# Kernel optimization log

Measured on AMD Instinct MI355X. Metric: run time of the kernel, lower is better.

## Reference

```python
import jax, jax.numpy as jnp
import numpy as np

B, T, D, H = 8, 1024, 512, 8
DK = D // H


def setup_inputs() -> dict:
    key = jax.random.key(0)
    ks = jax.random.split(key, 6)
    s = 0.02
    return {
        "inputs": jax.random.normal(ks[0], (B, T, D), jnp.float32),
        "ln1_g": jnp.ones((D,), jnp.float32),
        "ln1_b": jnp.zeros((D,), jnp.float32),
        "ln2_g": jnp.ones((D,), jnp.float32),
        "ln2_b": jnp.zeros((D,), jnp.float32),
        "W_qkv": jax.random.normal(ks[1], (3 * D, D), jnp.float32) * s,
        "W_pos": jax.random.normal(ks[2], (D, D), jnp.float32) * s,
        "W_out": jax.random.normal(ks[3], (D, D), jnp.float32) * s,
        "b_out": jnp.zeros((D,), jnp.float32),
        "pos_bias_u": jax.random.normal(ks[4], (H, DK), jnp.float32) * s,
        "pos_bias_v": jax.random.normal(ks[5], (H, DK), jnp.float32) * s,
    }


def layer_norm(x, g, b, eps=1e-5):
    mu = jnp.mean(x, axis=-1, keepdims=True)
    var = jnp.var(x, axis=-1, keepdims=True)
    return (x - mu) * jax.lax.rsqrt(var + eps) * g + b


def rel_shift(x):
    # x: (b, h, t1, t2); Transformer-XL pad-reshape-slice relative shift
    b, h, t1, t2 = x.shape
    xp = jnp.pad(x, ((0, 0), (0, 0), (0, 0), (1, 0)))  # zero col at front
    xp = xp.reshape(b, h, t2 + 1, t1)[:, :, 1:, :]
    return xp.reshape(b, h, t1, t2)


def reference(inputs, ln1_g, ln1_b, ln2_g, ln2_b, W_qkv, W_pos, W_out, b_out,
              pos_bias_u, pos_bias_v):
    b, t, d = inputs.shape
    # PositionalEmbedding: pos_seq is the literal data values inputs[0,:,0]
    pos_seq = inputs[0, :, 0]
    inv_freq = 1.0 / (10000.0 ** (jnp.arange(0, d, 2, dtype=jnp.float32) / d))
    sin_inp = pos_seq[:, None] * inv_freq[None, :]  # (T, D/2)
    pos_emb = jnp.concatenate([jnp.sin(sin_inp), jnp.cos(sin_inp)], axis=-1)  # (T, D)
    # outer layer norm, then inner layer norm inside forward_qkv
    x = layer_norm(inputs, ln1_g, ln1_b)
    xn = layer_norm(x, ln2_g, ln2_b)
    qkv = xn @ W_qkv.T  # (B, T, 3D)
    q, k, v = jnp.split(qkv, 3, axis=-1)
    q = q.reshape(b, t, H, DK)                       # (B, T, H, DK)
    k = k.reshape(b, t, H, DK).transpose(0, 2, 1, 3)  # (B, H, T, DK)
    v = v.reshape(b, t, H, DK).transpose(0, 2, 1, 3)  # (B, H, T, DK)
    p = (pos_emb @ W_pos.T).reshape(t, H, DK)         # (T, H, DK), pos batch = 1
    qu = (q + pos_bias_u).transpose(0, 2, 1, 3)       # (B, H, T, DK)
    qv = (q + pos_bias_v).transpose(0, 2, 1, 3)
    ac = jnp.einsum('bhqd,bhkd->bhqk', qu, k)
    bd = jnp.einsum('bhqd,khd->bhqk', qv, p)
    bd = rel_shift(bd)
    scores = (ac + bd) / jnp.sqrt(jnp.float32(DK))
    attn = jax.nn.softmax(scores, axis=-1)
    out = jnp.einsum('bhqk,bhkd->bqhd', attn, v).reshape(b, t, d)
    return out @ W_out.T + b_out
```

## Files before the change

kernel.cpp:

```cpp
#include <hip/hip_runtime.h>
#include <stdint.h>

#define B_ 8
#define T_ 1024
#define D_ 512
#define H_ 8
#define DK_ 64
#define M_ (B_*T_)

#define PREP_CAST_BLKS (5 * D_ * D_ / 4 / 256)
#define PREP_POS_BLKS  (T_)
#define PREP_LN_BLKS   (M_)
#define PREP_BLKS      (PREP_CAST_BLKS + PREP_POS_BLKS + PREP_LN_BLKS)

typedef unsigned short u16;
typedef __attribute__((ext_vector_type(8))) short bf16x8;
typedef __attribute__((ext_vector_type(4))) float f32x4;

static __device__ __forceinline__ u16 f2bf(float f) {
  union { float f; unsigned u; } v; v.f = f;
  unsigned r = (v.u + 0x7fffu + ((v.u >> 16) & 1u)) >> 16;
  return (u16)r;
}
static __device__ __forceinline__ u16 f2bf_ru(float f) {
  union { float f; unsigned u; } v; v.f = f;
  return (u16)((v.u + 0x8000u) >> 16);
}
static __device__ __forceinline__ float bf2f(u16 u) {
  union { unsigned u; float f; } v; v.u = ((unsigned)u) << 16;
  return v.f;
}
static __device__ __forceinline__ void async16(const u16* g, u16* l) {
  __builtin_amdgcn_global_load_lds(
      (const __attribute__((address_space(1))) void*)g,
      (__attribute__((address_space(3))) void*)l, 16, 0, 0);
}
static __device__ __forceinline__ f32x4 mfma16(bf16x8 a, bf16x8 b, f32x4 c) {
  return __builtin_amdgcn_mfma_f32_16x16x32_bf16(a, b, c, 0, 0, 0);
}

__global__ __launch_bounds__(256)
void prep_k(const float* __restrict__ wq, const float* __restrict__ wp,
            const float* __restrict__ wo, u16* __restrict__ dq,
            u16* __restrict__ dp, u16* __restrict__ dwo,
            const float* __restrict__ x, u16* __restrict__ pe,
            const float* __restrict__ g1, const float* __restrict__ b1,
            const float* __restrict__ g2, const float* __restrict__ b2,
            u16* __restrict__ xn) {
  __shared__ float red[16];
  const int blk = blockIdx.x;
  const int t = threadIdx.x;
  if (blk < PREP_CAST_BLKS) {
    const int na = 3 * D_ * D_ / 4, nb = D_ * D_ / 4;
    int i = blk * 256 + t;
    const float* s; u16* d; int j;
    if (i < na) { s = wq; d = dq; j = i; }
    else if (i < na + nb) { s = wp; d = dp; j = i - na; }
    else { s = wo; d = dwo; j = i - na - nb; }
    float4 v = ((const float4*)s)[j];
    ushort4 o;
    o.x = f2bf(v.x); o.y = f2bf(v.y); o.z = f2bf(v.z); o.w = f2bf(v.w);
    ((ushort4*)d)[j] = o;
  } else if (blk < PREP_CAST_BLKS + PREP_POS_BLKS) {
    const int tt = blk - PREP_CAST_BLKS;
    float pos = x[(size_t)tt * D_];
    float invf = expf(-(2.f * t / (float)D_) * 9.210340371976184f);
    float ang = pos * invf;
    pe[(size_t)tt * D_ + t] = f2bf(sinf(ang));
    pe[(size_t)tt * D_ + 256 + t] = f2bf(cosf(ang));
  } else {
    const int row = blk - PREP_CAST_BLKS - PREP_POS_BLKS;
    const float2 v = *(const float2*)(x + (size_t)row * D_ + t * 2);
    float a = v.x + v.y;
    float b = v.x * v.x + v.y * v.y;
    for (int off = 32; off; off >>= 1) { a += __shfl_down(a, off, 64); b += __shfl_down(b, off, 64); }
    if ((t & 63) == 0) { red[t >> 6] = a; red[8 + (t >> 6)] = b; }
    __syncthreads();
    a = red[0] + red[1] + red[2] + red[3];
    b = red[8] + red[9] + red[10] + red[11];
    float mu = a * (1.f / D_);
    float var = b * (1.f / D_) - mu * mu;
    float rs = rsqrtf(var + 1e-5f);
    const float2 g1v = *(const float2*)(g1 + t * 2);
    const float2 b1v = *(const float2*)(b1 + t * 2);
    float y0 = (v.x - mu) * rs * g1v.x + b1v.x;
    float y1 = (v.y - mu) * rs * g1v.y + b1v.y;
    __syncthreads();
    a = y0 + y1;
    b = y0 * y0 + y1 * y1;
    for (int off = 32; off; off >>= 1) { a += __shfl_down(a, off, 64); b += __shfl_down(b, off, 64); }
    if ((t & 63) == 0) { red[t >> 6] = a; red[8 + (t >> 6)] = b; }
    __syncthreads();
    a = red[0] + red[1] + red[2] + red[3];
    b = red[8] + red[9] + red[10] + red[11];
    mu = a * (1.f / D_);
    var = b * (1.f / D_) - mu * mu;
    rs = rsqrtf(var + 1e-5f);
    const float2 g2v = *(const float2*)(g2 + t * 2);
    const float2 b2v = *(const float2*)(b2 + t * 2);
    u16* o = xn + (size_t)row * D_ + t * 2;
    o[0] = f2bf((y0 - mu) * rs * g2v.x + b2v.x);
    o[1] = f2bf((y1 - mu) * rs * g2v.y + b2v.y);
  }
}

template<int MODE>
__global__ __launch_bounds__(256, 2)
void gemm_k(const u16* __restrict__ A, const u16* __restrict__ Bw,
            int M, int N, int K,
            u16* __restrict__ o0, u16* __restrict__ o1, u16* __restrict__ o2,
            float* __restrict__ fo, const float* __restrict__ bo) {
  __shared__ u16 As[2][128 * 32];
  __shared__ u16 Bs[2][128 * 32];
  const int tid = threadIdx.x;
  const int l = tid & 63, w = tid >> 6;
  const int m0 = blockIdx.x * 128, n0 = blockIdx.y * 128;
  const int wm = (w >> 1) * 64, wn = (w & 1) * 64;
  const int nk = K >> 5;

  auto stage = [&](int bufi, int kt) {
    const int row = tid >> 2;
    const int cg = ((tid & 3) ^ ((row + (row >> 2)) & 3)) * 8;
    const u16* ga = A + (size_t)(m0 + row) * K + kt * 32 + cg;
    u16* la = &As[bufi][tid * 8];
    async16(ga, la);
    async16(ga + (size_t)64 * K, la + 64 * 32);
    const u16* gb = Bw + (size_t)(n0 + row) * K + kt * 32 + cg;
    u16* lb = &Bs[bufi][tid * 8];
    async16(gb, lb);
    async16(gb + (size_t)64 * K, lb + 64 * 32);
  };

  const int fl = (((l & 15) + ((l & 15) >> 2)) & 3);
  const int coff = ((l >> 4) ^ fl) * 8;
  const int aoff = (l & 15) * 32 + coff;

  f32x4 acc[4][4] = {};
  stage(0, 0);
  for (int kt = 0; kt < nk; ++kt) {
    __syncthreads();
    if (kt + 1 < nk) stage((kt + 1) & 1, kt + 1);
    const u16* as = As[kt & 1];
    const u16* bs = Bs[kt & 1];
    bf16x8 af[4], bfr[4];
#pragma unroll
    for (int i = 0; i < 4; ++i)
      af[i] = *(const bf16x8*)&as[(wm + i * 16) * 32 + aoff];
#pragma unroll
    for (int j = 0; j < 4; ++j)
      bfr[j] = *(const bf16x8*)&bs[(wn + j * 16) * 32 + aoff];
#pragma unroll
    for (int i = 0; i < 4; ++i)
#pragma unroll
      for (int j = 0; j < 4; ++j)
        acc[i][j] = mfma16(af[i], bfr[j], acc[i][j]);
  }

#pragma unroll
  for (int i = 0; i < 4; ++i)
#pragma unroll
    for (int j = 0; j < 4; ++j) {
      const int row0 = m0 + wm + i * 16 + ((l >> 4) << 2);
      const int col = n0 + wn + j * 16 + (l & 15);
      if (MODE == 0) {
        const int sec = col >> 9, cc = col & 511;
        const int hh = cc >> 6, dk = cc & 63;
        const int bb = row0 >> 10, t0r = row0 & 1023;
        if (sec == 2) {
          ushort4 v4;
          v4.x = f2bf(acc[i][j][0]); v4.y = f2bf(acc[i][j][1]);
          v4.z = f2bf(acc[i][j][2]); v4.w = f2bf(acc[i][j][3]);
          *(ushort4*)&o2[((size_t)(bb * H_ + hh) * DK_ + dk) * T_ + t0r] = v4;
        } else {
          u16* dst = (sec == 0) ? o0 : o1;
#pragma unroll
          for (int r = 0; r < 4; ++r)
            dst[((size_t)(bb * H_ + hh) * T_ + t0r + r) * DK_ + dk] = f2bf(acc[i][j][r]);
        }
      } else if (MODE == 1) {
        const int hh = col >> 6, dk = col & 63;
#pragma unroll
        for (int r = 0; r < 4; ++r)
          o0[((size_t)hh * T_ + row0 + r) * DK_ + dk] = f2bf(acc[i][j][r]);
      } else {
#pragma unroll
        for (int r = 0; r < 4; ++r)
          fo[(size_t)(row0 + r) * D_ + col] = acc[i][j][r] + bo[col];
      }
    }
}

__global__ __launch_bounds__(256, 3)
void attn_k(const u16* __restrict__ q, const u16* __restrict__ kb,
            const u16* __restrict__ vt, const u16* __restrict__ pb,
            const float* __restrict__ bu, const float* __restrict__ bv,
            u16* __restrict__ ao) {
  __shared__ u16 k_lds[64 * 64];
  __shared__ u16 v_lds[64 * 64];
  __shared__ u16 p_lds[128 * 64];
  __shared__ u16 pscr[4][16 * 72];

  const int tid = threadIdx.x;
  const int l = tid & 63, w = tid >> 6;
  const int dd = blockIdx.x;
  const int bh = (dd & 7) * 8 + (dd >> 7);
  const int qb = (dd >> 3) & 15;
  const int q0 = qb * 64;
  const int b = bh >> 3, h = bh & 7;

  const u16* qB = q + (size_t)bh * T_ * DK_;
  const u16* kB = kb + (size_t)bh * T_ * DK_;
  const u16* vB = vt + (size_t)bh * DK_ * T_;
  const u16* pB = pb + (size_t)h * T_ * DK_;

  const float SCALE = 0.125f * 1.4426950408889634f;

  bf16x8 quf[2], qvf[2], qsf[2];
  {
    const float* buH = bu + h * DK_;
    const float* bvH = bv + h * DK_;
    const int row = q0 + w * 16 + (l & 15);
    const int row2 = (row + 1 < T_) ? row + 1 : T_ - 1;
    const int ko = (l >> 4) * 8;
    const bf16x8 qa0 = *(const bf16x8*)(qB + (size_t)row * DK_ + ko);
    const bf16x8 qa1 = *(const bf16x8*)(qB + (size_t)row * DK_ + ko + 32);
    const bf16x8 qs0 = *(const bf16x8*)(qB + (size_t)row2 * DK_ + ko);
    const bf16x8 qs1 = *(const bf16x8*)(qB + (size_t)row2 * DK_ + ko + 32);
#pragma unroll
    for (int jj = 0; jj < 8; ++jj) {
      float f0 = bf2f((u16)qa0[jj]), f1 = bf2f((u16)qa1[jj]);
      float g0 = bf2f((u16)qs0[jj]), g1 = bf2f((u16)qs1[jj]);
      float u0 = buH[ko + jj], u1 = buH[ko + 32 + jj];
      float v0 = bvH[ko + jj], v1 = bvH[ko + 32 + jj];
      quf[0][jj] = (short)f2bf((f0 + u0) * SCALE);
      quf[1][jj] = (short)f2bf((f1 + u1) * SCALE);
      qvf[0][jj] = (short)f2bf((f0 + v0) * SCALE);
      qvf[1][jj] = (short)f2bf((f1 + v1) * SCALE);
      qsf[0][jj] = (short)f2bf((g0 + v0) * SCALE);
      qsf[1][jj] = (short)f2bf((g1 + v1) * SCALE);
    }
  }

  f32x4 o[4] = {};
  float lrun[4] = {0.f, 0.f, 0.f, 0.f};
  float sv[4][4];

  const int rbase = 48 - w * 16;
  u16* pwv = &pscr[w][0];
  const int lrow = l & 15;
  const int c0s = ((l >> 4) ^ (l & 7)) * 8;
  const int c1s = c0s ^ 32;
  const int qrow0 = (l >> 4) * 4;

  int srcb[4], hi[4];
#pragma unroll
  for (int r = 0; r < 4; ++r) {
    int d = lrow - qrow0 - r + 15;
    srcb[r] = (((l >> 4) * 16 + (d & 15)) << 2);
    hi[r] = d >> 4;
  }

  const int rr0 = tid >> 3;
  const int cb = (tid & 7) * 8;
  const int swz = ((tid & 7) ^ (rr0 & 7)) * 8;
  const int wkv = rr0 * 64 + swz;

  uint4 kreg0, kreg1, vreg0, vreg1, preg0, preg1, preg2, preg3;
  auto loadKV = [&](int k0n) {
    kreg0 = *(const uint4*)(kB + (size_t)(k0n + rr0) * DK_ + cb);
    kreg1 = *(const uint4*)(kB + (size_t)(k0n + rr0 + 32) * DK_ + cb);
    vreg0 = *(const uint4*)(vB + (size_t)rr0 * T_ + k0n + cb);
    vreg1 = *(const uint4*)(vB + (size_t)(rr0 + 32) * T_ + k0n + cb);
  };
  auto pclamp = [&](int j) { return j < 0 ? 0 : (j > T_ - 1 ? T_ - 1 : j); };
  auto loadP = [&](int jb) {
    preg0 = *(const uint4*)(pB + (size_t)pclamp(jb + rr0) * DK_ + cb);
    preg1 = *(const uint4*)(pB + (size_t)pclamp(jb + 32 + rr0) * DK_ + cb);
    preg2 = *(const uint4*)(pB + (size_t)pclamp(jb + 64 + rr0) * DK_ + cb);
    preg3 = *(const uint4*)(pB + (size_t)pclamp(jb + 96 + rr0) * DK_ + cb);
  };

  loadKV(0);
  loadP(T_ - 64 - q0);

  for (int it = 0; it <= 16; ++it) {
    const int kt = it - (it > qb ? 1 : 0);
    const bool phaseU = (it > qb);
    const bool repeat = (it == qb + 1);
    const bool partial = (it == qb);
    const bool needMask = (it >= qb) && (it <= qb + 2);
    const int k0 = kt * 64;

    __syncthreads();
    if (!repeat) {
      *(uint4*)&k_lds[wkv] = kreg0;
      *(uint4*)&k_lds[wkv + 32 * 64] = kreg1;
      *(uint4*)&v_lds[wkv] = vreg0;
      *(uint4*)&v_lds[wkv + 32 * 64] = vreg1;
    }
    *(uint4*)&p_lds[wkv] = preg0;
    *(uint4*)&p_lds[wkv + 32 * 64] = preg1;
    *(uint4*)&p_lds[wkv + 64 * 64] = preg2;
    *(uint4*)&p_lds[wkv + 96 * 64] = preg3;
    asm volatile("s_waitcnt lgkmcnt(0)" ::: "memory");
    __builtin_amdgcn_sched_barrier(0);
    __builtin_amdgcn_s_barrier();
    __builtin_amdgcn_sched_barrier(0);

    if (it < 16) {
      if (it != qb) loadKV((it + 1 - (it + 1 > qb ? 1 : 0)) * 64);
      const bool pU = (it + 1 > qb);
      const int ktn = it + 1 - (pU ? 1 : 0);
      loadP(pU ? ktn * 64 - q0 - 65 : T_ - 64 + ktn * 64 - q0);
    }

    if (!repeat) {
      __builtin_amdgcn_s_setprio(1);
#pragma unroll
      for (int nf = 0; nf < 4; ++nf) {
        const u16* kb0 = &k_lds[(nf * 16 + lrow) * 64];
        bf16x8 b0 = *(const bf16x8*)(kb0 + c0s);
        bf16x8 b1 = *(const bf16x8*)(kb0 + c1s);
        f32x4 acs = {};
        acs = mfma16(quf[0], b0, acs);
        acs = mfma16(quf[1], b1, acs);
#pragma unroll
        for (int r = 0; r < 4; ++r) sv[nf][r] = acs[r];
      }
      __builtin_amdgcn_s_setprio(0);
    }

    {
      bf16x8 A0, A1;
      if (phaseU) { A0 = qsf[0]; A1 = qsf[1]; } else { A0 = qvf[0]; A1 = qvf[1]; }
      f32x4 c[5];
      __builtin_amdgcn_s_setprio(1);
#pragma unroll
      for (int fu = 0; fu < 5; ++fu) {
        const u16* pb0 = &p_lds[(rbase + fu * 16 + lrow) * 64];
        bf16x8 p0 = *(const bf16x8*)(pb0 + c0s);
        bf16x8 p1 = *(const bf16x8*)(pb0 + c1s);
        f32x4 cc = {};
        cc = mfma16(A0, p0, cc);
        cc = mfma16(A1, p1, cc);
        c[fu] = cc;
      }
      __builtin_amdgcn_s_setprio(0);
#pragma unroll
      for (int r = 0; r < 4; ++r) {
        float rot[6];
#pragma unroll
        for (int fu = 0; fu < 5; ++fu)
          rot[fu] = __int_as_float(
              __builtin_amdgcn_ds_bpermute(srcb[r], __float_as_int(c[fu][r])));
        rot[5] = 0.f;
#pragma unroll
        for (int nf = 0; nf < 4; ++nf) {
          float bd = hi[r] ? rot[nf + 1] : rot[nf];
          if (needMask) {
            int rel = (k0 + nf * 16 + lrow) - (q0 + w * 16 + qrow0 + r);
            bool ok = phaseU ? (rel >= 2) : (rel <= 0);
            bd = ok ? bd : 0.f;
          }
          sv[nf][r] += bd;
        }
      }
    }

    if (!partial) {
#pragma unroll
      for (int nf = 0; nf < 4; ++nf)
#pragma unroll
        for (int r = 0; r < 4; ++r)
          sv[nf][r] = __builtin_amdgcn_exp2f(sv[nf][r]);
#pragma unroll
      for (int r = 0; r < 4; ++r)
        lrun[r] += (sv[0][r] + sv[1][r]) + (sv[2][r] + sv[3][r]);

#pragma unroll
      for (int nf = 0; nf < 4; ++nf)
#pragma unroll
        for (int r = 0; r < 4; ++r)
          pwv[(qrow0 + r) * 72 + nf * 16 + lrow] = f2bf_ru(sv[nf][r]);

      bf16x8 pa0 = *(const bf16x8*)&pwv[lrow * 72 + (l >> 4) * 8];
      bf16x8 pa1 = *(const bf16x8*)&pwv[lrow * 72 + 32 + (l >> 4) * 8];
      __builtin_amdgcn_s_setprio(1);
#pragma unroll
      for (int df = 0; df < 4; ++df) {
        const u16* vb2 = &v_lds[(df * 16 + lrow) * 64];
        bf16x8 v0 = *(const bf16x8*)(vb2 + c0s);
        bf16x8 v1 = *(const bf16x8*)(vb2 + c1s);
        o[df] = mfma16(pa0, v0, o[df]);
        o[df] = mfma16(pa1, v1, o[df]);
      }
      __builtin_amdgcn_s_setprio(0);
    }
  }

#pragma unroll
  for (int r = 0; r < 4; ++r) {
#pragma unroll
    for (int off = 1; off < 16; off <<= 1) lrun[r] += __shfl_xor(lrun[r], off, 64);
    lrun[r] = 1.f / lrun[r];
  }
#pragma unroll
  for (int df = 0; df < 4; ++df)
#pragma unroll
    for (int r = 0; r < 4; ++r) {
      int qq = q0 + w * 16 + (l >> 4) * 4 + r;
      int dk = df * 16 + (l & 15);
      float val = o[df][r] * lrun[r];
      ao[((size_t)b * T_ + qq) * D_ + h * DK_ + dk] = f2bf(val);
    }
}

extern "C" void kernel_launch(void* const* d_in, const int* in_sizes, int n_in,
                              void* d_out, int out_size, void* d_ws, size_t ws_size,
                              hipStream_t stream) {
  const float* inputs = (const float*)d_in[0];
  const float* ln1_g = (const float*)d_in[1];
  const float* ln1_b = (const float*)d_in[2];
  const float* ln2_g = (const float*)d_in[3];
  const float* ln2_b = (const float*)d_in[4];
  const float* W_qkv = (const float*)d_in[5];
  const float* W_pos = (const float*)d_in[6];
  const float* W_out = (const float*)d_in[7];
  const float* b_out = (const float*)d_in[8];
  const float* pbu = (const float*)d_in[9];
  const float* pbv = (const float*)d_in[10];
  float* out = (float*)d_out;

  char* ws = (char*)d_ws;
  size_t off = 0;
  auto alloc = [&](size_t bytes) {
    char* p = ws + off;
    off += (bytes + 255) & ~(size_t)255;
    return p;
  };
  u16* xn   = (u16*)alloc((size_t)M_ * D_ * 2);
  u16* wqkv = (u16*)alloc((size_t)3 * D_ * D_ * 2);
  u16* wpos = (u16*)alloc((size_t)D_ * D_ * 2);
  u16* wout = (u16*)alloc((size_t)D_ * D_ * 2);
  u16* pemb = (u16*)alloc((size_t)T_ * D_ * 2);
  u16* qB   = (u16*)alloc((size_t)M_ * D_ * 2);
  u16* kbB  = (u16*)alloc((size_t)M_ * D_ * 2);
  u16* vtB  = (u16*)alloc((size_t)M_ * D_ * 2);
  u16* pbuf = (u16*)alloc((size_t)H_ * T_ * DK_ * 2);
  u16* aoB  = (u16*)alloc((size_t)M_ * D_ * 2);
  if (ws_size < off) return;

  prep_k<<<PREP_BLKS, 256, 0, stream>>>(W_qkv, W_pos, W_out, wqkv, wpos, wout,
                                        inputs, pemb, ln1_g, ln1_b, ln2_g, ln2_b, xn);
  gemm_k<1><<<dim3(T_ / 128, D_ / 128), 256, 0, stream>>>(
      pemb, wpos, T_, D_, D_, pbuf, nullptr, nullptr, nullptr, nullptr);
  gemm_k<0><<<dim3(M_ / 128, (3 * D_) / 128), 256, 0, stream>>>(
      xn, wqkv, M_, 3 * D_, D_, qB, kbB, vtB, nullptr, nullptr);
  attn_k<<<1024, 256, 0, stream>>>(qB, kbB, vtB, pbuf, pbu, pbv, aoB);
  gemm_k<2><<<dim3(M_ / 128, D_ / 128), 256, 0, stream>>>(
      aoB, wout, M_, D_, D_, nullptr, nullptr, nullptr, out, b_out);
}
```

Measured before the change: 137.4 us.

## Process 128 query rows per attention block sharing K/V and positional tiles

The attention kernel now uses 512-thread blocks covering two 64-row query tiles, so each K/V tile and a merged 192-row positional window are loaded once and shared by eight waves. The old extra repeat iteration for the diagonal tile is replaced by a separate extra positional buffer that the matching half of the waves process only on their transition tile. Positional-row clamping is dropped in favour of an offset base pointer, and the grid is halved. This is meant to cut global-load and barrier overhead per query row, at the cost of more shared memory per block, larger barriers, and possible wave imbalance on transition tiles.

```diff
diff --git a/kernel.cpp b/kernel.cpp
--- a/kernel.cpp
+++ b/kernel.cpp
@@ -190,28 +190,31 @@
     }
 }
 
-__global__ __launch_bounds__(256, 3)
+__global__ __launch_bounds__(512, 4)
 void attn_k(const u16* __restrict__ q, const u16* __restrict__ kb,
             const u16* __restrict__ vt, const u16* __restrict__ pb,
             const float* __restrict__ bu, const float* __restrict__ bv,
             u16* __restrict__ ao) {
   __shared__ u16 k_lds[64 * 64];
   __shared__ u16 v_lds[64 * 64];
-  __shared__ u16 p_lds[128 * 64];
-  __shared__ u16 pscr[4][16 * 72];
+  __shared__ u16 pm_lds[192 * 64];
+  __shared__ u16 px_lds[128 * 64];
+  __shared__ u16 pscr[8][16 * 72];
 
   const int tid = threadIdx.x;
   const int l = tid & 63, w = tid >> 6;
   const int dd = blockIdx.x;
-  const int bh = (dd & 7) * 8 + (dd >> 7);
-  const int qb = (dd >> 3) & 15;
-  const int q0 = qb * 64;
+  const int bh = (dd & 7) * 8 + ((dd >> 3) & 7);
+  const int qg = dd >> 6;
+  const int q0 = qg * 128;
+  const int qbA = qg * 2, qbB = qg * 2 + 1;
   const int b = bh >> 3, h = bh & 7;
+  const int diagKt = qbA + (w >> 2);
 
   const u16* qB = q + (size_t)bh * T_ * DK_;
   const u16* kB = kb + (size_t)bh * T_ * DK_;
   const u16* vB = vt + (size_t)bh * DK_ * T_;
-  const u16* pB = pb + (size_t)h * T_ * DK_;
+  const u16* pB2 = pb + (size_t)h * T_ * DK_ - 65 * DK_;
 
   const float SCALE = 0.125f * 1.4426950408889634f;
 
@@ -245,7 +248,8 @@
   float lrun[4] = {0.f, 0.f, 0.f, 0.f};
   float sv[4][4];
 
-  const int rbase = 48 - w * 16;
+  const int rbase = 112 - w * 16;
+  const int rbaseX = 48 - (w & 3) * 16;
   u16* pwv = &pscr[w][0];
   const int lrow = l & 15;
   const int c0s = ((l >> 4) ^ (l & 7)) * 8;
@@ -260,61 +264,64 @@
     hi[r] = d >> 4;
   }
 
-  const int rr0 = tid >> 3;
+  const int rr = tid >> 3;
   const int cb = (tid & 7) * 8;
-  const int swz = ((tid & 7) ^ (rr0 & 7)) * 8;
-  const int wkv = rr0 * 64 + swz;
-
-  uint4 kreg0, kreg1, vreg0, vreg1, preg0, preg1, preg2, preg3;
-  auto loadKV = [&](int k0n) {
-    kreg0 = *(const uint4*)(kB + (size_t)(k0n + rr0) * DK_ + cb);
-    kreg1 = *(const uint4*)(kB + (size_t)(k0n + rr0 + 32) * DK_ + cb);
-    vreg0 = *(const uint4*)(vB + (size_t)rr0 * T_ + k0n + cb);
-    vreg1 = *(const uint4*)(vB + (size_t)(rr0 + 32) * T_ + k0n + cb);
+  const int swz = ((tid & 7) ^ (rr & 7)) * 8;
+  const int wdst = rr * 64 + swz;
+  const unsigned kOffE = (unsigned)(rr * DK_ + cb);
+  const unsigned vOffE = (unsigned)(rr * T_ + cb);
+
+  uint4 kreg, vreg, pm0, pm1, pm2, px0, px1;
+  auto loadK = [&](int t) { kreg = *(const uint4*)(kB + kOffE + (unsigned)(t * 64 * DK_)); };
+  auto loadV = [&](int t) { vreg = *(const uint4*)(vB + vOffE + (unsigned)(t * 64)); };
+  auto loadPM = [&](int jb) {
+    const unsigned base = kOffE + (unsigned)((jb + 65) * DK_);
+    pm0 = *(const uint4*)(pB2 + base);
+    pm1 = *(const uint4*)(pB2 + base + 64u * DK_);
+    pm2 = *(const uint4*)(pB2 + base + 128u * DK_);
   };
-  auto pclamp = [&](int j) { return j < 0 ? 0 : (j > T_ - 1 ? T_ - 1 : j); };
-  auto loadP = [&](int jb) {
-    preg0 = *(const uint4*)(pB + (size_t)pclamp(jb + rr0) * DK_ + cb);
-    preg1 = *(const uint4*)(pB + (size_t)pclamp(jb + 32 + rr0) * DK_ + cb);
-    preg2 = *(const uint4*)(pB + (size_t)pclamp(jb + 64 + rr0) * DK_ + cb);
-    preg3 = *(const uint4*)(pB + (size_t)pclamp(jb + 96 + rr0) * DK_ + cb);
+  auto loadPX = [&](int jb) {
+    const unsigned base = kOffE + (unsigned)((jb + 65) * DK_);
+    px0 = *(const uint4*)(pB2 + base);
+    px1 = *(const uint4*)(pB2 + base + 64u * DK_);
   };
-
-  loadKV(0);
-  loadP(T_ - 64 - q0);
-
-  for (int it = 0; it <= 16; ++it) {
-    const int kt = it - (it > qb ? 1 : 0);
-    const bool phaseU = (it > qb);
-    const bool repeat = (it == qb + 1);
-    const bool partial = (it == qb);
-    const bool needMask = (it >= qb) && (it <= qb + 2);
+  auto mainJb = [&](int t) {
+    return (t <= qbA) ? (T_ - 128 + t * 64 - q0) : (t * 64 - q0 - 129);
+  };
+
+  loadK(0); loadV(0); loadPM(mainJb(0));
+  if (qbA == 0) loadPX(-65);
+
+  for (int kt = 0; kt < 16; ++kt) {
+    const bool transA = (kt == qbA), transB = (kt == qbB);
+    const bool mainLower = (kt <= qbA);
+    const bool mainMask = mainLower ? (kt == diagKt) : (kt <= diagKt + 1);
+    const bool myExtra = (transA && w < 4) || (transB && w >= 4);
     const int k0 = kt * 64;
 
     __syncthreads();
-    if (!repeat) {
-      *(uint4*)&k_lds[wkv] = kreg0;
-      *(uint4*)&k_lds[wkv + 32 * 64] = kreg1;
-      *(uint4*)&v_lds[wkv] = vreg0;
-      *(uint4*)&v_lds[wkv + 32 * 64] = vreg1;
-    }
-    *(uint4*)&p_lds[wkv] = preg0;
-    *(uint4*)&p_lds[wkv + 32 * 64] = preg1;
-    *(uint4*)&p_lds[wkv + 64 * 64] = preg2;
-    *(uint4*)&p_lds[wkv + 96 * 64] = preg3;
+    *(uint4*)&k_lds[wdst] = kreg;
+    *(uint4*)&v_lds[wdst] = vreg;
+    *(uint4*)&pm_lds[wdst] = pm0;
+    *(uint4*)&pm_lds[wdst + 64 * 64] = pm1;
+    *(uint4*)&pm_lds[wdst + 128 * 64] = pm2;
+    if (transA || transB) {
+      *(uint4*)&px_lds[wdst] = px0;
+      *(uint4*)&px_lds[wdst + 64 * 64] = px1;
+    }
     asm volatile("s_waitcnt lgkmcnt(0)" ::: "memory");
     __builtin_amdgcn_sched_barrier(0);
     __builtin_amdgcn_s_barrier();
     __builtin_amdgcn_sched_barrier(0);
 
-    if (it < 16) {
-      if (it != qb) loadKV((it + 1 - (it + 1 > qb ? 1 : 0)) * 64);
-      const bool pU = (it + 1 > qb);
-      const int ktn = it + 1 - (pU ? 1 : 0);
-      loadP(pU ? ktn * 64 - q0 - 65 : T_ - 64 + ktn * 64 - q0);
-    }
-
-    if (!repeat) {
+    if (kt < 15) {
+      const int t = kt + 1;
+      loadK(t); loadV(t); loadPM(mainJb(t));
+      if (t == qbA) loadPX(-65);
+      else if (t == qbB) loadPX(T_ - 64);
+    }
+
+    {
       __builtin_amdgcn_s_setprio(1);
 #pragma unroll
       for (int nf = 0; nf < 4; ++nf) {
@@ -332,12 +339,12 @@
 
     {
       bf16x8 A0, A1;
-      if (phaseU) { A0 = qsf[0]; A1 = qsf[1]; } else { A0 = qvf[0]; A1 = qvf[1]; }
+      if (mainLower) { A0 = qvf[0]; A1 = qvf[1]; } else { A0 = qsf[0]; A1 = qsf[1]; }
       f32x4 c[5];
       __builtin_amdgcn_s_setprio(1);
 #pragma unroll
       for (int fu = 0; fu < 5; ++fu) {
-        const u16* pb0 = &p_lds[(rbase + fu * 16 + lrow) * 64];
+        const u16* pb0 = &pm_lds[(rbase + fu * 16 + lrow) * 64];
         bf16x8 p0 = *(const bf16x8*)(pb0 + c0s);
         bf16x8 p1 = *(const bf16x8*)(pb0 + c1s);
         f32x4 cc = {};
@@ -348,18 +355,17 @@
       __builtin_amdgcn_s_setprio(0);
 #pragma unroll
       for (int r = 0; r < 4; ++r) {
-        float rot[6];
+        float rot[5];
 #pragma unroll
         for (int fu = 0; fu < 5; ++fu)
           rot[fu] = __int_as_float(
               __builtin_amdgcn_ds_bpermute(srcb[r], __float_as_int(c[fu][r])));
-        rot[5] = 0.f;
 #pragma unroll
         for (int nf = 0; nf < 4; ++nf) {
           float bd = hi[r] ? rot[nf + 1] : rot[nf];
-          if (needMask) {
+          if (mainMask) {
             int rel = (k0 + nf * 16 + lrow) - (q0 + w * 16 + qrow0 + r);
-            bool ok = phaseU ? (rel >= 2) : (rel <= 0);
+            bool ok = mainLower ? (rel <= 0) : (rel >= 2);
             bd = ok ? bd : 0.f;
           }
           sv[nf][r] += bd;
@@ -367,7 +373,40 @@
       }
     }
 
-    if (!partial) {
+    if (myExtra) {
+      bf16x8 A0, A1;
+      if (w < 4) { A0 = qsf[0]; A1 = qsf[1]; } else { A0 = qvf[0]; A1 = qvf[1]; }
+      f32x4 c[5];
+      __builtin_amdgcn_s_setprio(1);
+#pragma unroll
+      for (int fu = 0; fu < 5; ++fu) {
+        const u16* pb0 = &px_lds[(rbaseX + fu * 16 + lrow) * 64];
+        bf16x8 p0 = *(const bf16x8*)(pb0 + c0s);
+        bf16x8 p1 = *(const bf16x8*)(pb0 + c1s);
+        f32x4 cc = {};
+        cc = mfma16(A0, p0, cc);
+        cc = mfma16(A1, p1, cc);
+        c[fu] = cc;
+      }
+      __builtin_amdgcn_s_setprio(0);
+#pragma unroll
+      for (int r = 0; r < 4; ++r) {
+        float rot[5];
+#pragma unroll
+        for (int fu = 0; fu < 5; ++fu)
+          rot[fu] = __int_as_float(
+              __builtin_amdgcn_ds_bpermute(srcb[r], __float_as_int(c[fu][r])));
+#pragma unroll
+        for (int nf = 0; nf < 4; ++nf) {
+          float bd = hi[r] ? rot[nf + 1] : rot[nf];
+          int rel = (k0 + nf * 16 + lrow) - (q0 + w * 16 + qrow0 + r);
+          bool ok = (w < 4) ? (rel >= 2) : (rel <= 0);
+          sv[nf][r] += ok ? bd : 0.f;
+        }
+      }
+    }
+
+    {
 #pragma unroll
       for (int nf = 0; nf < 4; ++nf)
 #pragma unroll
@@ -456,7 +495,7 @@
       pemb, wpos, T_, D_, D_, pbuf, nullptr, nullptr, nullptr, nullptr);
   gemm_k<0><<<dim3(M_ / 128, (3 * D_) / 128), 256, 0, stream>>>(
       xn, wqkv, M_, 3 * D_, D_, qB, kbB, vtB, nullptr, nullptr);
-  attn_k<<<1024, 256, 0, stream>>>(qB, kbB, vtB, pbuf, pbu, pbv, aoB);
+  attn_k<<<512, 512, 0, stream>>>(qB, kbB, vtB, pbuf, pbu, pbv, aoB);
   gemm_k<2><<<dim3(M_ / 128, D_ / 128), 256, 0, stream>>>(
       aoB, wout, M_, D_, D_, nullptr, nullptr, nullptr, out, b_out);
 }
```

New measurement: 321.0 us. 2.34x slower.

## Double-buffer K/V/P tiles in LDS with async global-to-LDS loads

Applied to the files above, without the earlier changes.

Replaces register-staged prefetch of K, V and positional tiles with direct asynchronous global-to-LDS copies into double-buffered shared memory. The global reads now carry the XOR swizzle while LDS writes are linear. This removes the per-iteration LDS store phase and register pressure from staging, and keeps one barrier per step. The clamp on positional rows is dropped, so out-of-range rows are read unclamped. Shared memory roughly doubles and the occupancy hint of 3 is removed, which may lower occupancy.

```diff
diff --git a/kernel.cpp b/kernel.cpp
--- a/kernel.cpp
+++ b/kernel.cpp
@@ -190,14 +190,14 @@
     }
 }
 
-__global__ __launch_bounds__(256, 3)
+__global__ __launch_bounds__(256)
 void attn_k(const u16* __restrict__ q, const u16* __restrict__ kb,
             const u16* __restrict__ vt, const u16* __restrict__ pb,
             const float* __restrict__ bu, const float* __restrict__ bv,
             u16* __restrict__ ao) {
-  __shared__ u16 k_lds[64 * 64];
-  __shared__ u16 v_lds[64 * 64];
-  __shared__ u16 p_lds[128 * 64];
+  __shared__ u16 k_lds[2][64 * 64];
+  __shared__ u16 v_lds[2][64 * 64];
+  __shared__ u16 p_lds[2][128 * 64];
   __shared__ u16 pscr[4][16 * 72];
 
   const int tid = threadIdx.x;
@@ -211,7 +211,7 @@
   const u16* qB = q + (size_t)bh * T_ * DK_;
   const u16* kB = kb + (size_t)bh * T_ * DK_;
   const u16* vB = vt + (size_t)bh * DK_ * T_;
-  const u16* pB = pb + (size_t)h * T_ * DK_;
+  const u16* pB2 = pb + (size_t)h * T_ * DK_ - 65 * DK_;
 
   const float SCALE = 0.125f * 1.4426950408889634f;
 
@@ -261,29 +261,31 @@
   }
 
   const int rr0 = tid >> 3;
-  const int cb = (tid & 7) * 8;
-  const int swz = ((tid & 7) ^ (rr0 & 7)) * 8;
-  const int wkv = rr0 * 64 + swz;
-
-  uint4 kreg0, kreg1, vreg0, vreg1, preg0, preg1, preg2, preg3;
-  auto loadKV = [&](int k0n) {
-    kreg0 = *(const uint4*)(kB + (size_t)(k0n + rr0) * DK_ + cb);
-    kreg1 = *(const uint4*)(kB + (size_t)(k0n + rr0 + 32) * DK_ + cb);
-    vreg0 = *(const uint4*)(vB + (size_t)rr0 * T_ + k0n + cb);
-    vreg1 = *(const uint4*)(vB + (size_t)(rr0 + 32) * T_ + k0n + cb);
+  const int cg8 = ((tid & 7) ^ (rr0 & 7)) * 8;
+  const int dst0 = tid * 8;
+  const int pdst = rr0 * 64 + (tid & 7) * 8;
+
+  auto stageTile = [&](int itT) {
+    const int buf = itT & 1;
+    const int ktT = itT - (itT > qb ? 1 : 0);
+    const int k0n = ktT * 64;
+    const int jb = (itT > qb) ? (k0n - q0 - 65) : (T_ - 64 + k0n - q0);
+    const u16* gk = kB + (size_t)(k0n + rr0) * DK_ + cg8;
+    async16(gk, &k_lds[buf][dst0]);
+    async16(gk + 32 * DK_, &k_lds[buf][dst0 + 32 * 64]);
+    const u16* gv = vB + (size_t)rr0 * T_ + k0n + cg8;
+    async16(gv, &v_lds[buf][dst0]);
+    async16(gv + 32 * T_, &v_lds[buf][dst0 + 32 * 64]);
+    const u16* gp = pB2 + (size_t)(jb + 65 + rr0) * DK_ + cg8;
+#pragma unroll
+    for (int i = 0; i < 4; ++i)
+      async16(gp + (size_t)(i * 32) * DK_, &p_lds[buf][pdst + i * 32 * 64]);
   };
-  auto pclamp = [&](int j) { return j < 0 ? 0 : (j > T_ - 1 ? T_ - 1 : j); };
-  auto loadP = [&](int jb) {
-    preg0 = *(const uint4*)(pB + (size_t)pclamp(jb + rr0) * DK_ + cb);
-    preg1 = *(const uint4*)(pB + (size_t)pclamp(jb + 32 + rr0) * DK_ + cb);
-    preg2 = *(const uint4*)(pB + (size_t)pclamp(jb + 64 + rr0) * DK_ + cb);
-    preg3 = *(const uint4*)(pB + (size_t)pclamp(jb + 96 + rr0) * DK_ + cb);
-  };
-
-  loadKV(0);
-  loadP(T_ - 64 - q0);
+
+  stageTile(0);
 
   for (int it = 0; it <= 16; ++it) {
+    const int buf = it & 1;
     const int kt = it - (it > qb ? 1 : 0);
     const bool phaseU = (it > qb);
     const bool repeat = (it == qb + 1);
@@ -291,34 +293,22 @@
     const bool needMask = (it >= qb) && (it <= qb + 2);
     const int k0 = kt * 64;
 
-    __syncthreads();
-    if (!repeat) {
-      *(uint4*)&k_lds[wkv] = kreg0;
-      *(uint4*)&k_lds[wkv + 32 * 64] = kreg1;
-      *(uint4*)&v_lds[wkv] = vreg0;
-      *(uint4*)&v_lds[wkv + 32 * 64] = vreg1;
-    }
-    *(uint4*)&p_lds[wkv] = preg0;
-    *(uint4*)&p_lds[wkv + 32 * 64] = preg1;
-    *(uint4*)&p_lds[wkv + 64 * 64] = preg2;
-    *(uint4*)&p_lds[wkv + 96 * 64] = preg3;
-    asm volatile("s_waitcnt lgkmcnt(0)" ::: "memory");
+    asm volatile("s_waitcnt vmcnt(0)" ::: "memory");
     __builtin_amdgcn_sched_barrier(0);
     __builtin_amdgcn_s_barrier();
     __builtin_amdgcn_sched_barrier(0);
 
-    if (it < 16) {
-      if (it != qb) loadKV((it + 1 - (it + 1 > qb ? 1 : 0)) * 64);
-      const bool pU = (it + 1 > qb);
-      const int ktn = it + 1 - (pU ? 1 : 0);
-      loadP(pU ? ktn * 64 - q0 - 65 : T_ - 64 + ktn * 64 - q0);
-    }
+    if (it < 16) stageTile(it + 1);
+
+    const u16* kT = k_lds[buf];
+    const u16* vT = v_lds[buf];
+    const u16* pT = p_lds[buf];
 
     if (!repeat) {
       __builtin_amdgcn_s_setprio(1);
 #pragma unroll
       for (int nf = 0; nf < 4; ++nf) {
-        const u16* kb0 = &k_lds[(nf * 16 + lrow) * 64];
+        const u16* kb0 = &kT[(nf * 16 + lrow) * 64];
         bf16x8 b0 = *(const bf16x8*)(kb0 + c0s);
         bf16x8 b1 = *(const bf16x8*)(kb0 + c1s);
         f32x4 acs = {};
@@ -337,7 +327,7 @@
       __builtin_amdgcn_s_setprio(1);
 #pragma unroll
       for (int fu = 0; fu < 5; ++fu) {
-        const u16* pb0 = &p_lds[(rbase + fu * 16 + lrow) * 64];
+        const u16* pb0 = &pT[(rbase + fu * 16 + lrow) * 64];
         bf16x8 p0 = *(const bf16x8*)(pb0 + c0s);
         bf16x8 p1 = *(const bf16x8*)(pb0 + c1s);
         f32x4 cc = {};
@@ -348,12 +338,11 @@
       __builtin_amdgcn_s_setprio(0);
 #pragma unroll
       for (int r = 0; r < 4; ++r) {
-        float rot[6];
+        float rot[5];
 #pragma unroll
         for (int fu = 0; fu < 5; ++fu)
           rot[fu] = __int_as_float(
               __builtin_amdgcn_ds_bpermute(srcb[r], __float_as_int(c[fu][r])));
-        rot[5] = 0.f;
 #pragma unroll
         for (int nf = 0; nf < 4; ++nf) {
           float bd = hi[r] ? rot[nf + 1] : rot[nf];
@@ -388,7 +377,7 @@
       __builtin_amdgcn_s_setprio(1);
 #pragma unroll
       for (int df = 0; df < 4; ++df) {
-        const u16* vb2 = &v_lds[(df * 16 + lrow) * 64];
+        const u16* vb2 = &vT[(df * 16 + lrow) * 64];
         bf16x8 v0 = *(const bf16x8*)(vb2 + c0s);
         bf16x8 v1 = *(const bf16x8*)(vb2 + c1s);
         o[df] = mfma16(pa0, v0, o[df]);
```

Result: slower. 145.1 us (+5.6%).
